# Performance work log

Hardware: AMD Instinct MI355X
Metric: run time of the kernel (lower is better)

The kernel has to match this reference:

```python
import jax, jax.numpy as jnp
import numpy as np

BT, D, H = 128, 256, 512

def setup_inputs() -> dict:
    key = jax.random.key(0)
    ks = jax.random.split(key, 15)
    f = jnp.float32
    n = lambda k, s, sc=1.0: jax.random.normal(k, s, dtype=f) * sc
    return {
        "x_t": n(ks[0], (BT, D)),
        "h1": n(ks[1], (BT, H)), "h2": n(ks[2], (BT, H)),
        "mnu1": n(ks[3], (BT, H), 0.1), "mnu2": n(ks[4], (BT, H), 0.1),
        "mth1": n(ks[5], (BT, H), 0.1), "mth2": n(ks[6], (BT, H), 0.1),
        "mw11": n(ks[7], (BT, D, H), 0.01), "mw12": n(ks[8], (BT, D, H), 0.01),
        "mw21": n(ks[9], (BT, D, H), 0.01), "mw22": n(ks[10], (BT, D, H), 0.01),
        "w1": n(ks[11], (D, H), 1.0 / np.sqrt(D)),
        "w2": n(ks[12], (D, H), 1.0 / np.sqrt(D)),
        "nu_log": n(ks[13], (H,), 0.5),
        "theta_log": n(ks[14], (H,), 0.5),
    }

def reference(x_t, h1, h2, mnu1, mnu2, mth1, mth2, mw11, mw12, mw21, mw22, w1, w2, nu_log, theta_log):
    # Linear RTU parametrization: r = exp(-exp(nu)), theta = exp(theta_log), gamma = sqrt(1 - r^2)
    exp_nu = jnp.exp(nu_log)
    r = jnp.exp(-exp_nu)                       # (H,)
    theta = jnp.exp(theta_log)
    g = jnp.sqrt(1.0 - r * r)
    A = r * jnp.cos(theta)                     # rotation matrix entries (H,)
    B = r * jnp.sin(theta)
    xw1 = x_t @ w1                             # (Bt, H)
    xw2 = x_t @ w2
    # hidden state update (complex rotation recurrence)
    c1 = A * h1 - B * h2 + g * xw1
    c2 = B * h1 + A * h2 + g * xw2
    # parameter sensitivities of A, B, g
    dA_dnu = -A * exp_nu
    dB_dnu = -B * exp_nu
    dg_dnu = (r * r) * exp_nu / g
    dA_dth = -B * theta
    dB_dth = A * theta
    # RTRL eligibility traces wrt nu_log: (Bt, H)
    n1 = A * mnu1 - B * mnu2 + dA_dnu * h1 - dB_dnu * h2 + dg_dnu * xw1
    n2 = B * mnu1 + A * mnu2 + dB_dnu * h1 + dA_dnu * h2 + dg_dnu * xw2
    # traces wrt theta_log: (Bt, H)
    t1 = A * mth1 - B * mth2 + dA_dth * h1 - dB_dth * h2
    t2 = B * mth1 + A * mth2 + dB_dth * h1 + dA_dth * h2
    # traces wrt W1/W2: (Bt, D, H); direct term gamma * x outer delta
    gx = g * x_t[:, :, None]                   # (Bt, D, H)
    W11 = A * mw11 - B * mw12 + gx
    W12 = B * mw11 + A * mw12
    W21 = A * mw21 - B * mw22
    W22 = B * mw21 + A * mw22 + gx
    h_t = jax.nn.relu(jnp.concatenate((c1, c2), axis=-1))  # (Bt, 2H)
    return (h_t, c1, c2, n1, n2, t1, t2, W11, W12, W21, W22)
```

## Files before the change

### kernel.cpp

```cpp
#include <hip/hip_runtime.h>

#define BT 128
#define D  256
#define H  512

#define OFF_HT  0
#define OFF_C1  131072
#define OFF_C2  196608
#define OFF_N1  262144
#define OFF_N2  327680
#define OFF_T1  393216
#define OFF_T2  458752
#define OFF_W11 524288
#define OFF_W12 17301504
#define OFF_W21 34078720
#define OFF_W22 50855936

__global__ __launch_bounds__(256) void rtu_small(
    const float* __restrict__ x_t,
    const float* __restrict__ h1,  const float* __restrict__ h2,
    const float* __restrict__ mnu1, const float* __restrict__ mnu2,
    const float* __restrict__ mth1, const float* __restrict__ mth2,
    const float* __restrict__ w1,  const float* __restrict__ w2,
    const float* __restrict__ nu_log, const float* __restrict__ theta_log,
    float* __restrict__ out, float* __restrict__ ws)
{
    __shared__ float xs[D];
    const int tid = threadIdx.x;
    const int idx = blockIdx.x * 256 + tid;
    const int b   = idx >> 9;
    const int h   = idx & (H - 1);

    xs[tid] = x_t[b * D + tid];
    __syncthreads();

    const float nl = nu_log[h];
    const float tl = theta_log[h];
    const float exp_nu = expf(nl);
    const float r      = expf(-exp_nu);
    const float theta  = expf(tl);
    const float g      = sqrtf(fmaxf(1.0f - r * r, 0.0f));
    float s, c;
    sincosf(theta, &s, &c);
    const float A = r * c;
    const float B = r * s;
    const float dA_dnu = -A * exp_nu;
    const float dB_dnu = -B * exp_nu;
    const float dg_dnu = (r * r) * exp_nu / g;
    const float dA_dth = -B * theta;
    const float dB_dth =  A * theta;

    if (b == 0) {
        ws[h]            = A;
        ws[H + h]        = B;
        ws[2 * H + h]    = g;
    }

    float xw1 = 0.0f, xw2 = 0.0f;
    #pragma unroll 8
    for (int d = 0; d < D; ++d) {
        const float xv = xs[d];
        xw1 = fmaf(xv, w1[d * H + h], xw1);
        xw2 = fmaf(xv, w2[d * H + h], xw2);
    }

    const float h1v = h1[idx],  h2v = h2[idx];
    const float mn1 = mnu1[idx], mn2 = mnu2[idx];
    const float mt1 = mth1[idx], mt2 = mth2[idx];

    const float c1v = A * h1v - B * h2v + g * xw1;
    const float c2v = B * h1v + A * h2v + g * xw2;

    const float n1v = A * mn1 - B * mn2 + dA_dnu * h1v - dB_dnu * h2v + dg_dnu * xw1;
    const float n2v = B * mn1 + A * mn2 + dB_dnu * h1v + dA_dnu * h2v + dg_dnu * xw2;

    const float t1v = A * mt1 - B * mt2 + dA_dth * h1v - dB_dth * h2v;
    const float t2v = B * mt1 + A * mt2 + dB_dth * h1v + dA_dth * h2v;

    out[OFF_HT + b * (2 * H) + h]     = fmaxf(c1v, 0.0f);
    out[OFF_HT + b * (2 * H) + H + h] = fmaxf(c2v, 0.0f);
    out[OFF_C1 + idx] = c1v;
    out[OFF_C2 + idx] = c2v;
    out[OFF_N1 + idx] = n1v;
    out[OFF_N2 + idx] = n2v;
    out[OFF_T1 + idx] = t1v;
    out[OFF_T2 + idx] = t2v;
}

__global__ __launch_bounds__(256) void rtu_big(
    const float4* __restrict__ mw11, const float4* __restrict__ mw12,
    const float4* __restrict__ mw21, const float4* __restrict__ mw22,
    const float* __restrict__ x_t,
    const float* __restrict__ ws,
    float* __restrict__ out)
{
    const int e  = blockIdx.x * 256 + threadIdx.x;
    const int hq = e & 127;
    const int bd = e >> 7;

    const float x = x_t[bd];

    const float4 A4 = ((const float4*)(ws))[hq];
    const float4 B4 = ((const float4*)(ws + H))[hq];
    const float4 g4 = ((const float4*)(ws + 2 * H))[hq];

    const float4 m11 = mw11[e];
    const float4 m12 = mw12[e];
    const float4 m21 = mw21[e];
    const float4 m22 = mw22[e];

    float4 o11, o12, o21, o22;

    const float gx_x = g4.x * x, gx_y = g4.y * x, gx_z = g4.z * x, gx_w = g4.w * x;

    o11.x = fmaf(A4.x, m11.x, fmaf(-B4.x, m12.x, gx_x));
    o11.y = fmaf(A4.y, m11.y, fmaf(-B4.y, m12.y, gx_y));
    o11.z = fmaf(A4.z, m11.z, fmaf(-B4.z, m12.z, gx_z));
    o11.w = fmaf(A4.w, m11.w, fmaf(-B4.w, m12.w, gx_w));

    o12.x = fmaf(B4.x, m11.x, A4.x * m12.x);
    o12.y = fmaf(B4.y, m11.y, A4.y * m12.y);
    o12.z = fmaf(B4.z, m11.z, A4.z * m12.z);
    o12.w = fmaf(B4.w, m11.w, A4.w * m12.w);

    o21.x = fmaf(A4.x, m21.x, -B4.x * m22.x);
    o21.y = fmaf(A4.y, m21.y, -B4.y * m22.y);
    o21.z = fmaf(A4.z, m21.z, -B4.z * m22.z);
    o21.w = fmaf(A4.w, m21.w, -B4.w * m22.w);

    o22.x = fmaf(B4.x, m21.x, fmaf(A4.x, m22.x, gx_x));
    o22.y = fmaf(B4.y, m21.y, fmaf(A4.y, m22.y, gx_y));
    o22.z = fmaf(B4.z, m21.z, fmaf(A4.z, m22.z, gx_z));
    o22.w = fmaf(B4.w, m21.w, fmaf(A4.w, m22.w, gx_w));

    ((float4*)(out + OFF_W11))[e] = o11;
    ((float4*)(out + OFF_W12))[e] = o12;
    ((float4*)(out + OFF_W21))[e] = o21;
    ((float4*)(out + OFF_W22))[e] = o22;
}

extern "C" void kernel_launch(void* const* d_in, const int* in_sizes, int n_in,
                              void* d_out, int out_size, void* d_ws, size_t ws_size,
                              hipStream_t stream) {
    const float* x_t   = (const float*)d_in[0];
    const float* h1    = (const float*)d_in[1];
    const float* h2    = (const float*)d_in[2];
    const float* mnu1  = (const float*)d_in[3];
    const float* mnu2  = (const float*)d_in[4];
    const float* mth1  = (const float*)d_in[5];
    const float* mth2  = (const float*)d_in[6];
    const float* mw11  = (const float*)d_in[7];
    const float* mw12  = (const float*)d_in[8];
    const float* mw21  = (const float*)d_in[9];
    const float* mw22  = (const float*)d_in[10];
    const float* w1    = (const float*)d_in[11];
    const float* w2    = (const float*)d_in[12];
    const float* nu_log    = (const float*)d_in[13];
    const float* theta_log = (const float*)d_in[14];

    float* out = (float*)d_out;
    float* ws  = (float*)d_ws;

    rtu_small<<<(BT * H) / 256, 256, 0, stream>>>(
        x_t, h1, h2, mnu1, mnu2, mth1, mth2, w1, w2, nu_log, theta_log, out, ws);

    rtu_big<<<(BT * D * H / 4) / 256, 256, 0, stream>>>(
        (const float4*)mw11, (const float4*)mw12, (const float4*)mw21,
        (const float4*)mw22, x_t, ws, out);
}
```

Measured before the change: 484.6 us.

## Fuse small and big kernels into one launch with per-block coefficient recompute

Merges the two kernels into one launch. The first 256 blocks do the small matmul and state update, and the remaining blocks do the large trace update. Big-path blocks now recompute A, B and g for all H into shared memory instead of reading them from a workspace written by the first kernel. This removes the kernel-launch boundary and the serial dependency, so the small work overlaps with the bandwidth-bound stream. The cost is redundant transcendental math in every one of the 16384 big blocks, plus a barrier before each block streams.

```diff
diff --git a/kernel.cpp b/kernel.cpp
--- a/kernel.cpp
+++ b/kernel.cpp
@@ -16,102 +16,113 @@
 #define OFF_W21 34078720
 #define OFF_W22 50855936
 
-__global__ __launch_bounds__(256) void rtu_small(
-    const float* __restrict__ x_t,
-    const float* __restrict__ h1,  const float* __restrict__ h2,
-    const float* __restrict__ mnu1, const float* __restrict__ mnu2,
-    const float* __restrict__ mth1, const float* __restrict__ mth2,
-    const float* __restrict__ w1,  const float* __restrict__ w2,
-    const float* __restrict__ nu_log, const float* __restrict__ theta_log,
-    float* __restrict__ out, float* __restrict__ ws)
+#define SMALL_BLOCKS 256
+#define BIG_BLOCKS   16384
+
+__global__ __launch_bounds__(256) void rtu_fused(
+    const float*  __restrict__ x_t,
+    const float*  __restrict__ h1,   const float* __restrict__ h2,
+    const float*  __restrict__ mnu1, const float* __restrict__ mnu2,
+    const float*  __restrict__ mth1, const float* __restrict__ mth2,
+    const float4* __restrict__ mw11, const float4* __restrict__ mw12,
+    const float4* __restrict__ mw21, const float4* __restrict__ mw22,
+    const float*  __restrict__ w1,   const float* __restrict__ w2,
+    const float*  __restrict__ nu_log, const float* __restrict__ theta_log,
+    float* __restrict__ out)
 {
+    __shared__ float sA[H];
+    __shared__ float sB[H];
+    __shared__ float sG[H];
     __shared__ float xs[D];
+
     const int tid = threadIdx.x;
-    const int idx = blockIdx.x * 256 + tid;
-    const int b   = idx >> 9;
-    const int h   = idx & (H - 1);
 
-    xs[tid] = x_t[b * D + tid];
+    if (blockIdx.x < SMALL_BLOCKS) {
+        const int idx = blockIdx.x * 256 + tid;
+        const int b   = idx >> 9;
+        const int h   = idx & (H - 1);
+
+        xs[tid] = x_t[b * D + tid];
+        __syncthreads();
+
+        const float exp_nu = expf(nu_log[h]);
+        const float r      = expf(-exp_nu);
+        const float theta  = expf(theta_log[h]);
+        const float g      = sqrtf(fmaxf(1.0f - r * r, 0.0f));
+        float s, c;
+        sincosf(theta, &s, &c);
+        const float A = r * c;
+        const float B = r * s;
+        const float dA_dnu = -A * exp_nu;
+        const float dB_dnu = -B * exp_nu;
+        const float dg_dnu = (r * r) * exp_nu / g;
+        const float dA_dth = -B * theta;
+        const float dB_dth =  A * theta;
+
+        float xw1 = 0.0f, xw2 = 0.0f;
+        #pragma unroll 8
+        for (int d = 0; d < D; ++d) {
+            const float xv = xs[d];
+            xw1 = fmaf(xv, w1[d * H + h], xw1);
+            xw2 = fmaf(xv, w2[d * H + h], xw2);
+        }
+
+        const float h1v = h1[idx],  h2v = h2[idx];
+        const float mn1 = mnu1[idx], mn2 = mnu2[idx];
+        const float mt1 = mth1[idx], mt2 = mth2[idx];
+
+        const float c1v = A * h1v - B * h2v + g * xw1;
+        const float c2v = B * h1v + A * h2v + g * xw2;
+
+        const float n1v = A * mn1 - B * mn2 + dA_dnu * h1v - dB_dnu * h2v + dg_dnu * xw1;
+        const float n2v = B * mn1 + A * mn2 + dB_dnu * h1v + dA_dnu * h2v + dg_dnu * xw2;
+
+        const float t1v = A * mt1 - B * mt2 + dA_dth * h1v - dB_dth * h2v;
+        const float t2v = B * mt1 + A * mt2 + dB_dth * h1v + dA_dth * h2v;
+
+        out[OFF_HT + b * (2 * H) + h]     = fmaxf(c1v, 0.0f);
+        out[OFF_HT + b * (2 * H) + H + h] = fmaxf(c2v, 0.0f);
+        out[OFF_C1 + idx] = c1v;
+        out[OFF_C2 + idx] = c2v;
+        out[OFF_N1 + idx] = n1v;
+        out[OFF_N2 + idx] = n2v;
+        out[OFF_T1 + idx] = t1v;
+        out[OFF_T2 + idx] = t2v;
+        return;
+    }
+
+    #pragma unroll
+    for (int i = 0; i < 2; ++i) {
+        const int h = tid + i * 256;
+        const float exp_nu = expf(nu_log[h]);
+        const float r      = expf(-exp_nu);
+        const float theta  = expf(theta_log[h]);
+        float s, c;
+        sincosf(theta, &s, &c);
+        sA[h] = r * c;
+        sB[h] = r * s;
+        sG[h] = sqrtf(fmaxf(1.0f - r * r, 0.0f));
+    }
     __syncthreads();
 
-    const float nl = nu_log[h];
-    const float tl = theta_log[h];
-    const float exp_nu = expf(nl);
-    const float r      = expf(-exp_nu);
-    const float theta  = expf(tl);
-    const float g      = sqrtf(fmaxf(1.0f - r * r, 0.0f));
-    float s, c;
-    sincosf(theta, &s, &c);
-    const float A = r * c;
-    const float B = r * s;
-    const float dA_dnu = -A * exp_nu;
-    const float dB_dnu = -B * exp_nu;
-    const float dg_dnu = (r * r) * exp_nu / g;
-    const float dA_dth = -B * theta;
-    const float dB_dth =  A * theta;
-
-    if (b == 0) {
-        ws[h]            = A;
-        ws[H + h]        = B;
-        ws[2 * H + h]    = g;
-    }
-
-    float xw1 = 0.0f, xw2 = 0.0f;
-    #pragma unroll 8
-    for (int d = 0; d < D; ++d) {
-        const float xv = xs[d];
-        xw1 = fmaf(xv, w1[d * H + h], xw1);
-        xw2 = fmaf(xv, w2[d * H + h], xw2);
-    }
-
-    const float h1v = h1[idx],  h2v = h2[idx];
-    const float mn1 = mnu1[idx], mn2 = mnu2[idx];
-    const float mt1 = mth1[idx], mt2 = mth2[idx];
-
-    const float c1v = A * h1v - B * h2v + g * xw1;
-    const float c2v = B * h1v + A * h2v + g * xw2;
-
-    const float n1v = A * mn1 - B * mn2 + dA_dnu * h1v - dB_dnu * h2v + dg_dnu * xw1;
-    const float n2v = B * mn1 + A * mn2 + dB_dnu * h1v + dA_dnu * h2v + dg_dnu * xw2;
-
-    const float t1v = A * mt1 - B * mt2 + dA_dth * h1v - dB_dth * h2v;
-    const float t2v = B * mt1 + A * mt2 + dB_dth * h1v + dA_dth * h2v;
-
-    out[OFF_HT + b * (2 * H) + h]     = fmaxf(c1v, 0.0f);
-    out[OFF_HT + b * (2 * H) + H + h] = fmaxf(c2v, 0.0f);
-    out[OFF_C1 + idx] = c1v;
-    out[OFF_C2 + idx] = c2v;
-    out[OFF_N1 + idx] = n1v;
-    out[OFF_N2 + idx] = n2v;
-    out[OFF_T1 + idx] = t1v;
-    out[OFF_T2 + idx] = t2v;
-}
-
-__global__ __launch_bounds__(256) void rtu_big(
-    const float4* __restrict__ mw11, const float4* __restrict__ mw12,
-    const float4* __restrict__ mw21, const float4* __restrict__ mw22,
-    const float* __restrict__ x_t,
-    const float* __restrict__ ws,
-    float* __restrict__ out)
-{
-    const int e  = blockIdx.x * 256 + threadIdx.x;
+    const int e  = (blockIdx.x - SMALL_BLOCKS) * 256 + tid;
     const int hq = e & 127;
     const int bd = e >> 7;
 
     const float x = x_t[bd];
 
-    const float4 A4 = ((const float4*)(ws))[hq];
-    const float4 B4 = ((const float4*)(ws + H))[hq];
-    const float4 g4 = ((const float4*)(ws + 2 * H))[hq];
+    const float4 A4 = ((const float4*)sA)[hq];
+    const float4 B4 = ((const float4*)sB)[hq];
+    const float4 g4 = ((const float4*)sG)[hq];
 
     const float4 m11 = mw11[e];
     const float4 m12 = mw12[e];
     const float4 m21 = mw21[e];
     const float4 m22 = mw22[e];
 
+    const float gx_x = g4.x * x, gx_y = g4.y * x, gx_z = g4.z * x, gx_w = g4.w * x;
+
     float4 o11, o12, o21, o22;
-
-    const float gx_x = g4.x * x, gx_y = g4.y * x, gx_z = g4.z * x, gx_w = g4.w * x;
 
     o11.x = fmaf(A4.x, m11.x, fmaf(-B4.x, m12.x, gx_x));
     o11.y = fmaf(A4.y, m11.y, fmaf(-B4.y, m12.y, gx_y));
@@ -159,12 +170,10 @@
     const float* theta_log = (const float*)d_in[14];
 
     float* out = (float*)d_out;
-    float* ws  = (float*)d_ws;
 
-    rtu_small<<<(BT * H) / 256, 256, 0, stream>>>(
-        x_t, h1, h2, mnu1, mnu2, mth1, mth2, w1, w2, nu_log, theta_log, out, ws);
-
-    rtu_big<<<(BT * D * H / 4) / 256, 256, 0, stream>>>(
-        (const float4*)mw11, (const float4*)mw12, (const float4*)mw21,
-        (const float4*)mw22, x_t, ws, out);
+    rtu_fused<<<SMALL_BLOCKS + BIG_BLOCKS, 256, 0, stream>>>(
+        x_t, h1, h2, mnu1, mnu2, mth1, mth2,
+        (const float4*)mw11, (const float4*)mw12,
+        (const float4*)mw21, (const float4*)mw22,
+        w1, w2, nu_log, theta_log, out);
 }
```

Result: faster. 464.3 us (-4.2%).
